# Kernel optimization log

Hardware: AMD Instinct MI355X
Metric: run time of the kernel (lower is better)

## Reference

```python
import jax, jax.numpy as jnp
import numpy as np

N_HEADS = 16
D_MODEL = 1024
D_K = D_MODEL // N_HEADS


def setup_inputs() -> dict:
    key = jax.random.key(0)
    ks = jax.random.split(key, 7)
    B, S = 2, 2048
    init = 0.02
    return {
        "query": jax.random.normal(ks[0], (B, S, D_MODEL), dtype=jnp.float32),
        "key": jax.random.normal(ks[1], (B, S, D_MODEL), dtype=jnp.float32),
        "value": jax.random.normal(ks[2], (B, S, D_MODEL), dtype=jnp.float32),
        "W_q": jax.random.normal(ks[3], (D_MODEL, D_MODEL), dtype=jnp.float32) * init,
        "W_k": jax.random.normal(ks[4], (D_MODEL, D_MODEL), dtype=jnp.float32) * init,
        "W_v": jax.random.normal(ks[5], (D_MODEL, D_MODEL), dtype=jnp.float32) * init,
        "W_o": jax.random.normal(ks[6], (D_MODEL, D_MODEL), dtype=jnp.float32) * init,
    }


def _split_heads(x):
    # (B, S, d_model) -> (B, H, S, d_k)
    B, S, _ = x.shape
    return x.reshape(B, S, N_HEADS, D_K).transpose(0, 2, 1, 3)


def reference(query, key, value, W_q, W_k, W_v, W_o):
    scale = jnp.sqrt(jnp.asarray(D_K, dtype=query.dtype))
    # torch Linear: y = x @ W.T
    Q = _split_heads(query @ W_q.T)   # (B,H,Sq,dk)
    K = _split_heads(key @ W_k.T)     # (B,H,Sk,dk)
    V = _split_heads(value @ W_v.T)   # (B,H,Sk,dk)
    scores = jnp.einsum("bhqd,bhkd->bhqk", Q, K) / scale
    attn = jax.nn.softmax(scores, axis=-1)           # (B,H,Sq,Sk); dropout p=0 -> identity
    attn_weights = attn.mean(axis=1)                 # (B,Sq,Sk) interpretable weights
    head_out = jnp.einsum("bhqk,bhkd->bqhd", attn, V)  # (B,Sq,H,dk)
    # NOTE: the original computes a head-gating (W_h) whose result is overwritten
    # by the concat below -> dead code, omitted.
    B, Sq = head_out.shape[0], head_out.shape[1]
    out = head_out.reshape(B, Sq, D_MODEL) @ W_o.T   # (B,Sq,d_model)
    return (out, attn_weights)
```

## Files before the change

### kernel.cpp

```cpp
#include <hip/hip_runtime.h>
#include <hip/hip_bf16.h>

#define Bq 2
#define Hh 16
#define Ss 2048
#define Dm 1024
#define Dk 64
#define SCALE 0.125f

typedef _Float16 f16x8 __attribute__((ext_vector_type(8)));
typedef _Float16 f16x4 __attribute__((ext_vector_type(4)));
typedef float    f32x4 __attribute__((ext_vector_type(4)));


__device__ __forceinline__ void gl_lds16(const void* g, void* lds) {
    __builtin_amdgcn_global_load_lds(
        (const __attribute__((address_space(1))) void*)g,
        (__attribute__((address_space(3))) void*)lds, 16, 0, 0);
}

__global__ __launch_bounds__(256) void convert_kernel(
    const float* __restrict__ q, const float* __restrict__ k,
    const float* __restrict__ v, const float* __restrict__ wq,
    const float* __restrict__ wk, const float* __restrict__ wv,
    const float* __restrict__ wo,
    _Float16* __restrict__ qd, _Float16* __restrict__ kd,
    _Float16* __restrict__ vd, _Float16* __restrict__ wd)
{
    int seg = blockIdx.y;
    const float* src; _Float16* dst; int n4;
    switch (seg) {
        case 0: src = q; dst = qd; n4 = 1048576; break;
        case 1: src = k; dst = kd; n4 = 1048576; break;
        case 2: src = v; dst = vd; n4 = 1048576; break;
        default:
            src = (seg == 3) ? wq : (seg == 4) ? wk : (seg == 5) ? wv : wo;
            dst = wd + (size_t)(seg - 3) * 1048576;
            n4 = 262144;
    }
    for (int i = blockIdx.x * 256 + threadIdx.x; i < n4; i += gridDim.x * 256) {
        float4 x = ((const float4*)src)[i];
        f16x4 h = {(_Float16)x.x, (_Float16)x.y, (_Float16)x.z, (_Float16)x.w};
        ((f16x4*)dst)[i] = h;
    }
}

__global__ __launch_bounds__(256) void gemm_qkv(
    const _Float16* __restrict__ qf, const _Float16* __restrict__ kf,
    const _Float16* __restrict__ vf, const _Float16* __restrict__ Wh,
    _Float16* __restrict__ Qd, _Float16* __restrict__ Kd,
    _Float16* __restrict__ Vd)
{
    __shared__ _Float16 As[128 * 32];
    __shared__ _Float16 Ws[128 * 32];
    int z = blockIdx.z;
    const _Float16* A = (z == 0) ? qf : (z == 1) ? kf : vf;
    const _Float16* W = Wh + (size_t)z * (Dm * Dm);
    int t = threadIdx.x, lane = t & 63, w = t >> 6;
    int quad = lane >> 4, l15 = lane & 15;
    int wm = w & 1, wn = w >> 1;
    int n0 = blockIdx.x * 128, m0 = blockIdx.y * 128;

    f32x4 acc[4][4] = {};
    for (int k0 = 0; k0 < Dm; k0 += 32) {
        __syncthreads();
        for (int j = 0; j < 2; ++j) {
            int ca = w * 128 + j * 64 + lane;
            int row = ca >> 2, c8 = (ca & 3) * 8;
            gl_lds16(&A[(size_t)(m0 + row) * Dm + k0 + c8],
                     &As[(size_t)(w * 128 + j * 64) * 8]);
            gl_lds16(&W[(size_t)(n0 + row) * Dm + k0 + c8],
                     &Ws[(size_t)(w * 128 + j * 64) * 8]);
        }
        __syncthreads();
        f16x8 af[4], bf[4];
        for (int mi = 0; mi < 4; ++mi)
            af[mi] = *(const f16x8*)&As[(wm * 64 + mi * 16 + l15) * 32 + quad * 8];
        for (int ni = 0; ni < 4; ++ni)
            bf[ni] = *(const f16x8*)&Ws[(wn * 64 + ni * 16 + l15) * 32 + quad * 8];
        for (int mi = 0; mi < 4; ++mi)
            for (int ni = 0; ni < 4; ++ni)
                acc[mi][ni] = __builtin_amdgcn_mfma_f32_16x16x32_f16(
                    af[mi], bf[ni], acc[mi][ni], 0, 0, 0);
    }
    _Float16* Y = (z == 0) ? Qd : (z == 1) ? Kd : Vd;
    for (int mi = 0; mi < 4; ++mi)
        for (int ni = 0; ni < 4; ++ni)
            for (int r = 0; r < 4; ++r) {
                int m = m0 + wm * 64 + mi * 16 + quad * 4 + r;
                int n = n0 + wn * 64 + ni * 16 + l15;
                int b = m >> 11, s = m & (Ss - 1);
                int h = n >> 6,  d = n & 63;
                _Float16 v = (_Float16)acc[mi][ni][r];
                if (z < 2)
                    Y[(((size_t)(b * Hh + h) * Ss + s) << 6) + d] = v;
                else
                    Y[((size_t)(b * Hh + h) * Dk + d) * Ss + s] = v;
            }
}

__global__ __launch_bounds__(256) void gemm_out(
    const _Float16* __restrict__ HO, const _Float16* __restrict__ Woh,
    float* __restrict__ out)
{
    __shared__ _Float16 As[128 * 32];
    __shared__ _Float16 Ws[64 * 32];
    int t = threadIdx.x, lane = t & 63, w = t >> 6;
    int quad = lane >> 4, l15 = lane & 15;
    int n0 = blockIdx.x * 64, m0 = blockIdx.y * 128;

    f32x4 acc[2][4] = {};
    for (int k0 = 0; k0 < Dm; k0 += 32) {
        __syncthreads();
        for (int j = 0; j < 2; ++j) {
            int ca = w * 128 + j * 64 + lane;
            int row = ca >> 2, c8 = (ca & 3) * 8;
            gl_lds16(&HO[(size_t)(m0 + row) * Dm + k0 + c8],
                     &As[(size_t)(w * 128 + j * 64) * 8]);
        }
        {
            int cw = w * 64 + lane;
            int row = cw >> 2, c8 = (cw & 3) * 8;
            gl_lds16(&Woh[(size_t)(n0 + row) * Dm + k0 + c8],
                     &Ws[(size_t)(w * 64) * 8]);
        }
        __syncthreads();
        f16x8 af[2], bf[4];
        for (int mi = 0; mi < 2; ++mi)
            af[mi] = *(const f16x8*)&As[(w * 32 + mi * 16 + l15) * 32 + quad * 8];
        for (int ni = 0; ni < 4; ++ni)
            bf[ni] = *(const f16x8*)&Ws[(ni * 16 + l15) * 32 + quad * 8];
        for (int mi = 0; mi < 2; ++mi)
            for (int ni = 0; ni < 4; ++ni)
                acc[mi][ni] = __builtin_amdgcn_mfma_f32_16x16x32_f16(
                    af[mi], bf[ni], acc[mi][ni], 0, 0, 0);
    }
    for (int mi = 0; mi < 2; ++mi)
        for (int ni = 0; ni < 4; ++ni)
            for (int r = 0; r < 4; ++r) {
                int m = m0 + w * 32 + mi * 16 + quad * 4 + r;
                int n = n0 + ni * 16 + l15;
                out[(size_t)m * Dm + n] = acc[mi][ni][r];
            }
}

__global__ __launch_bounds__(256) void flash_kernel(
    const _Float16* __restrict__ Qh, const _Float16* __restrict__ Kh,
    const _Float16* __restrict__ Vt, _Float16* __restrict__ HO,
    float* __restrict__ lw)
{
    __shared__ alignas(16) _Float16 Ks[64][72];
    __shared__ alignas(16) _Float16 Vs[64][72];
    __shared__ alignas(16) _Float16 Ps[4][16][72];
    int t = threadIdx.x;
    int lane = t & 63, w = t >> 6;
    int quad = lane >> 4, l15 = lane & 15;
    int bh = blockIdx.x;
    int q0 = blockIdx.y * 64;

    const _Float16* Qp = Qh + (size_t)bh * Ss * Dk;
    const _Float16* Kp = Kh + (size_t)bh * Ss * Dk;
    const _Float16* Vp = Vt + (size_t)bh * Dk * Ss;

    f16x8 qf0 = *(const f16x8*)&Qp[(size_t)(q0 + w * 16 + l15) * Dk + quad * 8];
    f16x8 qf1 = *(const f16x8*)&Qp[(size_t)(q0 + w * 16 + l15) * Dk + 32 + quad * 8];

    f32x4 o_acc[4] = {};
    float lsum[4] = {0.f, 0.f, 0.f, 0.f};

    for (int kt = 0; kt < Ss / 64; ++kt) {
        __syncthreads();
        for (int i = 0; i < 2; ++i) {
            int e = i * 256 + t; int row = e >> 3, col = (e & 7) * 8;
            *(f16x8*)&Ks[row][col] =
                *(const f16x8*)&Kp[(size_t)(kt * 64 + row) * Dk + col];
            *(f16x8*)&Vs[row][col] =
                *(const f16x8*)&Vp[(size_t)row * Ss + kt * 64 + col];
        }
        __syncthreads();

        for (int nt = 0; nt < 4; ++nt) {
            f16x8 b0 = *(const f16x8*)&Ks[nt * 16 + l15][quad * 8];
            f16x8 b1 = *(const f16x8*)&Ks[nt * 16 + l15][32 + quad * 8];
            f32x4 z = {};
            z = __builtin_amdgcn_mfma_f32_16x16x32_f16(qf0, b0, z, 0, 0, 0);
            z = __builtin_amdgcn_mfma_f32_16x16x32_f16(qf1, b1, z, 0, 0, 0);
            for (int r = 0; r < 4; ++r) {
                float p = __expf(z[r] * SCALE);
                lsum[r] += p;
                Ps[w][quad * 4 + r][nt * 16 + l15] = (_Float16)p;
            }
        }
        f16x8 pf0 = *(const f16x8*)&Ps[w][l15][quad * 8];
        f16x8 pf1 = *(const f16x8*)&Ps[w][l15][32 + quad * 8];
        for (int dt = 0; dt < 4; ++dt) {
            f16x8 v0 = *(const f16x8*)&Vs[dt * 16 + l15][quad * 8];
            f16x8 v1 = *(const f16x8*)&Vs[dt * 16 + l15][32 + quad * 8];
            o_acc[dt] = __builtin_amdgcn_mfma_f32_16x16x32_f16(pf0, v0, o_acc[dt], 0, 0, 0);
            o_acc[dt] = __builtin_amdgcn_mfma_f32_16x16x32_f16(pf1, v1, o_acc[dt], 0, 0, 0);
        }
    }

    for (int r = 0; r < 4; ++r)
        for (int msk = 1; msk < 16; msk <<= 1)
            lsum[r] += __shfl_xor(lsum[r], msk);

    int b = bh >> 4, h = bh & 15;
    float inv_l[4];
    for (int r = 0; r < 4; ++r) inv_l[r] = 1.0f / lsum[r];
    for (int dt = 0; dt < 4; ++dt)
        for (int r = 0; r < 4; ++r) {
            int q = q0 + w * 16 + quad * 4 + r;
            HO[((size_t)(b * Ss + q)) * Dm + h * Dk + dt * 16 + l15] =
                (_Float16)(o_acc[dt][r] * inv_l[r]);
        }
    if (l15 == 0)
        for (int r = 0; r < 4; ++r) {
            int q = q0 + w * 16 + quad * 4 + r;
            lw[(size_t)bh * Ss + q] = lsum[r];
        }
}

__global__ __launch_bounds__(256) void attn_mean_kernel(
    const _Float16* __restrict__ Qh, const _Float16* __restrict__ Kh,
    const float* __restrict__ lw, float* __restrict__ out_attn)
{
    __shared__ alignas(16) _Float16 Ks[64][72];
    int t = threadIdx.x;
    int lane = t & 63, w = t >> 6;
    int quad = lane >> 4, l15 = lane & 15;
    int k0 = blockIdx.x * 64;
    int q0 = blockIdx.y * 64;
    int b  = blockIdx.z;
    int qrow = q0 + w * 16;

    int srow0 = t >> 3, scol0 = (t & 7) * 8;
    int srow1 = (256 + t) >> 3, scol1 = scol0;

    f16x8 kr0, kr1, qn0, qn1;
    float4 ln;
    {
        size_t base = (size_t)(b * Hh) * Ss;
        kr0 = *(const f16x8*)&Kh[(base + k0 + srow0) * Dk + scol0];
        kr1 = *(const f16x8*)&Kh[(base + k0 + srow1) * Dk + scol1];
        qn0 = *(const f16x8*)&Qh[(base + qrow + l15) * Dk + quad * 8];
        qn1 = *(const f16x8*)&Qh[(base + qrow + l15) * Dk + 32 + quad * 8];
        ln  = *(const float4*)&lw[base + qrow + quad * 4];
    }

    f32x4 acc[4] = {};
    for (int h = 0; h < Hh; ++h) {
        __syncthreads();
        *(f16x8*)&Ks[srow0][scol0] = kr0;
        *(f16x8*)&Ks[srow1][scol1] = kr1;
        f16x8 qf0 = qn0, qf1 = qn1;
        float4 lv = ln;
        if (h < Hh - 1) {
            size_t base = (size_t)(b * Hh + h + 1) * Ss;
            kr0 = *(const f16x8*)&Kh[(base + k0 + srow0) * Dk + scol0];
            kr1 = *(const f16x8*)&Kh[(base + k0 + srow1) * Dk + scol1];
            qn0 = *(const f16x8*)&Qh[(base + qrow + l15) * Dk + quad * 8];
            qn1 = *(const f16x8*)&Qh[(base + qrow + l15) * Dk + 32 + quad * 8];
            ln  = *(const float4*)&lw[base + qrow + quad * 4];
        }
        __syncthreads();

        float ir[4] = {1.0f / lv.x, 1.0f / lv.y, 1.0f / lv.z, 1.0f / lv.w};
        for (int nt = 0; nt < 4; ++nt) {
            f16x8 b0 = *(const f16x8*)&Ks[nt * 16 + l15][quad * 8];
            f16x8 b1 = *(const f16x8*)&Ks[nt * 16 + l15][32 + quad * 8];
            f32x4 z = {};
            z = __builtin_amdgcn_mfma_f32_16x16x32_f16(qf0, b0, z, 0, 0, 0);
            z = __builtin_amdgcn_mfma_f32_16x16x32_f16(qf1, b1, z, 0, 0, 0);
            for (int r = 0; r < 4; ++r)
                acc[nt][r] += __expf(z[r] * SCALE) * ir[r];
        }
    }

    for (int nt = 0; nt < 4; ++nt)
        for (int r = 0; r < 4; ++r) {
            int q = qrow + quad * 4 + r;
            out_attn[((size_t)(b * Ss + q)) * Ss + k0 + nt * 16 + l15] =
                acc[nt][r] * (1.0f / Hh);
        }
}

extern "C" void kernel_launch(void* const* d_in, const int* in_sizes, int n_in,
                              void* d_out, int out_size, void* d_ws, size_t ws_size,
                              hipStream_t stream) {
    const float* query = (const float*)d_in[0];
    const float* key   = (const float*)d_in[1];
    const float* value = (const float*)d_in[2];
    const float* Wq    = (const float*)d_in[3];
    const float* Wk    = (const float*)d_in[4];
    const float* Wv    = (const float*)d_in[5];
    const float* Wo    = (const float*)d_in[6];

    float* out      = (float*)d_out;
    float* attn_out = out + (size_t)4194304;

    _Float16* HO = (_Float16*)attn_out;
    _Float16* qf = (_Float16*)(attn_out + 2097152);
    _Float16* kf = qf + 4194304;
    _Float16* vf = kf + 4194304;

    _Float16* Qh = (_Float16*)d_ws;
    _Float16* Kh = Qh + (size_t)4194304;
    _Float16* Vt = Kh + (size_t)4194304;
    _Float16* Wh = Vt + (size_t)4194304;
    float*    lw = (float*)(Wh + (size_t)4194304);

    convert_kernel<<<dim3(256, 7), 256, 0, stream>>>(
        query, key, value, Wq, Wk, Wv, Wo, qf, kf, vf, Wh);

    gemm_qkv<<<dim3(8, 32, 3), 256, 0, stream>>>(qf, kf, vf, Wh, Qh, Kh, Vt);

    flash_kernel<<<dim3(Bq * Hh, Ss / 64), 256, 0, stream>>>(Qh, Kh, Vt, HO, lw);

    gemm_out<<<dim3(16, 32), 256, 0, stream>>>(HO, Wh + (size_t)3 * 1048576, out);

    attn_mean_kernel<<<dim3(Ss / 64, Ss / 64, Bq), 256, 0, stream>>>(
        Qh, Kh, lw, attn_out);
}
```

Before: 303.5 us.

## Give each flash-attention wave 32 query rows and compute S transposed

Each wave now handles 32 query rows in two 16-row halves, so a block covers 128 queries and the grid along the sequence halves. Every K and V tile loaded into LDS is reused across twice as many queries, and V fragments are loaded once per tile and shared by both halves. The QK^T MFMA swaps its operands so each lane holds four consecutive keys for one query row. That allows vectorized f16x4 writes of P to LDS and a cheaper row-sum reduction at the end. In exchange there are fewer blocks (512) and more registers per thread, which may reduce occupancy.

New measurement: 308.7 us. No clear change (+1.7%).

```diff
diff --git a/kernel.cpp b/kernel.cpp
--- a/kernel.cpp
+++ b/kernel.cpp
@@ -151,22 +151,25 @@
 {
     __shared__ alignas(16) _Float16 Ks[64][72];
     __shared__ alignas(16) _Float16 Vs[64][72];
-    __shared__ alignas(16) _Float16 Ps[4][16][72];
+    __shared__ alignas(16) _Float16 Ps[4][32][72];
     int t = threadIdx.x;
     int lane = t & 63, w = t >> 6;
     int quad = lane >> 4, l15 = lane & 15;
     int bh = blockIdx.x;
-    int q0 = blockIdx.y * 64;
+    int q0 = blockIdx.y * 128 + w * 32;
 
     const _Float16* Qp = Qh + (size_t)bh * Ss * Dk;
     const _Float16* Kp = Kh + (size_t)bh * Ss * Dk;
     const _Float16* Vp = Vt + (size_t)bh * Dk * Ss;
 
-    f16x8 qf0 = *(const f16x8*)&Qp[(size_t)(q0 + w * 16 + l15) * Dk + quad * 8];
-    f16x8 qf1 = *(const f16x8*)&Qp[(size_t)(q0 + w * 16 + l15) * Dk + 32 + quad * 8];
-
-    f32x4 o_acc[4] = {};
-    float lsum[4] = {0.f, 0.f, 0.f, 0.f};
+    f16x8 qf[2][2];
+    for (int qh = 0; qh < 2; ++qh)
+        for (int kf = 0; kf < 2; ++kf)
+            qf[qh][kf] = *(const f16x8*)
+                &Qp[(size_t)(q0 + qh * 16 + l15) * Dk + kf * 32 + quad * 8];
+
+    f32x4 o_acc[2][4] = {};
+    float lsum[2] = {0.f, 0.f};
 
     for (int kt = 0; kt < Ss / 64; ++kt) {
         __syncthreads();
@@ -180,45 +183,58 @@
         __syncthreads();
 
         for (int nt = 0; nt < 4; ++nt) {
-            f16x8 b0 = *(const f16x8*)&Ks[nt * 16 + l15][quad * 8];
-            f16x8 b1 = *(const f16x8*)&Ks[nt * 16 + l15][32 + quad * 8];
-            f32x4 z = {};
-            z = __builtin_amdgcn_mfma_f32_16x16x32_f16(qf0, b0, z, 0, 0, 0);
-            z = __builtin_amdgcn_mfma_f32_16x16x32_f16(qf1, b1, z, 0, 0, 0);
+            f16x8 kf0 = *(const f16x8*)&Ks[nt * 16 + l15][quad * 8];
+            f16x8 kf1 = *(const f16x8*)&Ks[nt * 16 + l15][32 + quad * 8];
+            for (int qh = 0; qh < 2; ++qh) {
+                f32x4 z = {};
+                z = __builtin_amdgcn_mfma_f32_16x16x32_f16(kf0, qf[qh][0], z, 0, 0, 0);
+                z = __builtin_amdgcn_mfma_f32_16x16x32_f16(kf1, qf[qh][1], z, 0, 0, 0);
+                float p0 = __expf(z[0] * SCALE);
+                float p1 = __expf(z[1] * SCALE);
+                float p2 = __expf(z[2] * SCALE);
+                float p3 = __expf(z[3] * SCALE);
+                lsum[qh] += (p0 + p1) + (p2 + p3);
+                f16x4 hv = {(_Float16)p0, (_Float16)p1, (_Float16)p2, (_Float16)p3};
+                *(f16x4*)&Ps[w][qh * 16 + l15][nt * 16 + quad * 4] = hv;
+            }
+        }
+
+        f16x8 vf[4][2];
+        for (int dt = 0; dt < 4; ++dt) {
+            vf[dt][0] = *(const f16x8*)&Vs[dt * 16 + l15][quad * 8];
+            vf[dt][1] = *(const f16x8*)&Vs[dt * 16 + l15][32 + quad * 8];
+        }
+        for (int qh = 0; qh < 2; ++qh) {
+            f16x8 pf0 = *(const f16x8*)&Ps[w][qh * 16 + l15][quad * 8];
+            f16x8 pf1 = *(const f16x8*)&Ps[w][qh * 16 + l15][32 + quad * 8];
+            for (int dt = 0; dt < 4; ++dt) {
+                o_acc[qh][dt] = __builtin_amdgcn_mfma_f32_16x16x32_f16(
+                    pf0, vf[dt][0], o_acc[qh][dt], 0, 0, 0);
+                o_acc[qh][dt] = __builtin_amdgcn_mfma_f32_16x16x32_f16(
+                    pf1, vf[dt][1], o_acc[qh][dt], 0, 0, 0);
+            }
+        }
+    }
+
+    for (int qh = 0; qh < 2; ++qh) {
+        lsum[qh] += __shfl_xor(lsum[qh], 16);
+        lsum[qh] += __shfl_xor(lsum[qh], 32);
+    }
+
+    int b = bh >> 4, h = bh & 15;
+    for (int qh = 0; qh < 2; ++qh) {
+        float ir[4];
+        for (int r = 0; r < 4; ++r)
+            ir[r] = 1.0f / __shfl(lsum[qh], quad * 4 + r);
+        for (int dt = 0; dt < 4; ++dt)
             for (int r = 0; r < 4; ++r) {
-                float p = __expf(z[r] * SCALE);
-                lsum[r] += p;
-                Ps[w][quad * 4 + r][nt * 16 + l15] = (_Float16)p;
-            }
-        }
-        f16x8 pf0 = *(const f16x8*)&Ps[w][l15][quad * 8];
-        f16x8 pf1 = *(const f16x8*)&Ps[w][l15][32 + quad * 8];
-        for (int dt = 0; dt < 4; ++dt) {
-            f16x8 v0 = *(const f16x8*)&Vs[dt * 16 + l15][quad * 8];
-            f16x8 v1 = *(const f16x8*)&Vs[dt * 16 + l15][32 + quad * 8];
-            o_acc[dt] = __builtin_amdgcn_mfma_f32_16x16x32_f16(pf0, v0, o_acc[dt], 0, 0, 0);
-            o_acc[dt] = __builtin_amdgcn_mfma_f32_16x16x32_f16(pf1, v1, o_acc[dt], 0, 0, 0);
-        }
-    }
-
-    for (int r = 0; r < 4; ++r)
-        for (int msk = 1; msk < 16; msk <<= 1)
-            lsum[r] += __shfl_xor(lsum[r], msk);
-
-    int b = bh >> 4, h = bh & 15;
-    float inv_l[4];
-    for (int r = 0; r < 4; ++r) inv_l[r] = 1.0f / lsum[r];
-    for (int dt = 0; dt < 4; ++dt)
-        for (int r = 0; r < 4; ++r) {
-            int q = q0 + w * 16 + quad * 4 + r;
-            HO[((size_t)(b * Ss + q)) * Dm + h * Dk + dt * 16 + l15] =
-                (_Float16)(o_acc[dt][r] * inv_l[r]);
-        }
-    if (l15 == 0)
-        for (int r = 0; r < 4; ++r) {
-            int q = q0 + w * 16 + quad * 4 + r;
-            lw[(size_t)bh * Ss + q] = lsum[r];
-        }
+                int q = q0 + qh * 16 + quad * 4 + r;
+                HO[((size_t)(b * Ss + q)) * Dm + h * Dk + dt * 16 + l15] =
+                    (_Float16)(o_acc[qh][dt][r] * ir[r]);
+            }
+        if (lane < 16)
+            lw[(size_t)bh * Ss + q0 + qh * 16 + lane] = lsum[qh];
+    }
 }
 
 __global__ __launch_bounds__(256) void attn_mean_kernel(
@@ -315,7 +331,7 @@
 
     gemm_qkv<<<dim3(8, 32, 3), 256, 0, stream>>>(qf, kf, vf, Wh, Qh, Kh, Vt);
 
-    flash_kernel<<<dim3(Bq * Hh, Ss / 64), 256, 0, stream>>>(Qh, Kh, Vt, HO, lw);
+    flash_kernel<<<dim3(Bq * Hh, Ss / 128), 256, 0, stream>>>(Qh, Kh, Vt, HO, lw);
 
     gemm_out<<<dim3(16, 32), 256, 0, stream>>>(HO, Wh + (size_t)3 * 1048576, out);
 
```
